# Kernel tuning notes

Measured on AMD Instinct MI355X. Metric: run time of the kernel, lower is better.

The kernel has to match this reference:

```python
import jax, jax.numpy as jnp
import numpy as np

EPS_BN = 1e-5


def _batchnorm(h, g, b):
    # training-mode BatchNorm1d over the flattened (B*N*k) axis
    mu = jnp.mean(h, axis=0)
    var = jnp.var(h, axis=0)
    return g * (h - mu) * jax.lax.rsqrt(var + EPS_BN) + b


def setup_inputs() -> dict:
    key = jax.random.key(0)
    ks = jax.random.split(key, 5)
    B, N = 4, 8192
    x = jax.random.normal(ks[0], (B, N, 3), dtype=jnp.float32)
    W1 = jax.random.normal(ks[1], (7, 10), dtype=jnp.float32) * (1.0 / np.sqrt(7.0))
    b1 = jax.random.normal(ks[2], (10,), dtype=jnp.float32) * 0.01
    W2 = jax.random.normal(ks[3], (10, 10), dtype=jnp.float32) * (1.0 / np.sqrt(10.0))
    b2 = jax.random.normal(ks[4], (10,), dtype=jnp.float32) * 0.01
    g1 = jnp.ones((10,), jnp.float32); be1 = jnp.zeros((10,), jnp.float32)
    g2 = jnp.ones((10,), jnp.float32); be2 = jnp.zeros((10,), jnp.float32)
    return {"x": x, "W1": W1, "b1": b1, "g1": g1, "be1": be1,
            "W2": W2, "b2": b2, "g2": g2, "be2": be2, "k": 9}


def reference(x, W1, b1, g1, be1, W2, b2, g2, be2, k):
    B, N, C = x.shape
    # --- kNN graph (brute force, self included as nearest) ---
    sq = jnp.sum(x * x, axis=-1)                                    # (B,N)
    d2 = sq[:, :, None] + sq[:, None, :] - 2.0 * jnp.einsum('bnc,bmc->bnm', x, x)
    _, idx = jax.lax.top_k(-d2, k + 1)                              # (B,N,k+1)
    nbrs = x[jnp.arange(B)[:, None, None], idx]                     # (B,N,k+1,3)
    rel = (nbrs - x[:, :, None, :])[:, :, 1:, :]                    # drop self -> (B,N,k,3)
    # --- sort neighbors by azimuth phi = atan2(y, x) ---
    phi = jnp.arctan2(rel[..., 1], rel[..., 0])                     # (B,N,k)
    order = jnp.argsort(phi, axis=-1)
    v1 = jnp.take_along_axis(rel, order[..., None], axis=2)         # (B,N,k,3)
    v2 = jnp.roll(v1, -1, axis=2)                                   # next neighbor (cyclic)
    # --- umbrella-style surface features ---
    centroids = 0.5 * (v1 + v2)
    normals = jnp.cross(v1, v2)
    normals = normals / (jnp.linalg.norm(normals, axis=-1, keepdims=True) + 1e-6)
    sign = jnp.where(normals[..., 0:1, 0] > 0, 1.0, -1.0)[..., None]  # (B,N,1,1)
    normals = normals * sign
    position = jnp.sum(normals * centroids, axis=-1, keepdims=True) / jnp.sqrt(jnp.asarray(3.0, x.dtype))
    feat = jnp.concatenate([centroids, normals, position], axis=-1)   # (B,N,k,7)
    feat = feat.reshape(B * N * k, 7)
    # --- tiny MLP + max-pool over k ---
    h = jax.nn.relu(_batchnorm(feat @ W1 + b1, g1, be1))
    h = jax.nn.relu(_batchnorm(h @ W2 + b2, g2, be2))
    return jnp.max(h.reshape(B, N, k, 10), axis=2)                  # (B,N,10)
```

## Files before the change

kernel.cpp:

```cpp
#include <hip/hip_runtime.h>
#include <math.h>
#include <float.h>
#include <stdint.h>

#define B_ 4
#define N_ 8192
#define K_ 9
#define NPTS (B_ * N_)
#define NROWS (NPTS * K_)
#define SPLIT 8
#define CHUNK (N_ / SPLIT)
#define NGROUP 32
#define GSIZE (CHUNK / NGROUP)
#define GSTRIDE 33

__device__ __forceinline__ float dist2f(float4 q, float4 c) {
  float dot = q.x * c.x + q.y * c.y + q.z * c.z;
  return (q.w + c.w) - 2.0f * dot;
}

#define GDECL(G) float gd##G; int gi##G;
#define SCANG(G)                                                           \
  { float bgd = FLT_MAX; int bgi = 0;                                      \
    _Pragma("clang loop unroll(disable)")                                  \
    for (int jj = 0; jj < GSIZE; jj += 4) {                                \
      const float4* cp = CH + (G * GSTRIDE + jj);                          \
      float4 c0 = cp[0], c1 = cp[1], c2 = cp[2], c3 = cp[3];               \
      int j = G * GSIZE + jj;                                              \
      float d0 = dist2f(q, c0), d1 = dist2f(q, c1);                        \
      float d2 = dist2f(q, c2), d3 = dist2f(q, c3);                        \
      if (HS) {                                                            \
        d0 = (j + 0 == nl) ? FLT_MAX : d0;                                 \
        d1 = (j + 1 == nl) ? FLT_MAX : d1;                                 \
        d2 = (j + 2 == nl) ? FLT_MAX : d2;                                 \
        d3 = (j + 3 == nl) ? FLT_MAX : d3;                                 \
      }                                                                    \
      bool l0 = d0 < bgd; bgd = l0 ? d0 : bgd; bgi = l0 ? (j + 0) : bgi;   \
      bool l1 = d1 < bgd; bgd = l1 ? d1 : bgd; bgi = l1 ? (j + 1) : bgi;   \
      bool l2 = d2 < bgd; bgd = l2 ? d2 : bgd; bgi = l2 ? (j + 2) : bgi;   \
      bool l3 = d3 < bgd; bgd = l3 ? d3 : bgd; bgi = l3 ? (j + 3) : bgi;   \
    }                                                                      \
    gd##G = bgd; gi##G = bgi; }
#define LM(G)                                                              \
  { bool lt = gd##G < wd;                                                  \
    wd = lt ? gd##G : wd; wi = lt ? gi##G : wi; wg = lt ? G : wg; }
#define WBK(G)                                                             \
  { bool m = (wg == G); gd##G = m ? nd : gd##G; gi##G = m ? ni : gi##G; }

template <bool HS>
__device__ __forceinline__ void knn_chunk(const float4* CH, float4 q, int nl,
                                          int j0, int s, int p,
                                          uint2* __restrict__ PBDI) {
  GDECL(0) GDECL(1) GDECL(2) GDECL(3) GDECL(4) GDECL(5) GDECL(6) GDECL(7)
  GDECL(8) GDECL(9) GDECL(10) GDECL(11) GDECL(12) GDECL(13) GDECL(14) GDECL(15)
  GDECL(16) GDECL(17) GDECL(18) GDECL(19) GDECL(20) GDECL(21) GDECL(22) GDECL(23)
  GDECL(24) GDECL(25) GDECL(26) GDECL(27) GDECL(28) GDECL(29) GDECL(30) GDECL(31)

  SCANG(0) SCANG(1) SCANG(2) SCANG(3) SCANG(4) SCANG(5) SCANG(6) SCANG(7)
  SCANG(8) SCANG(9) SCANG(10) SCANG(11) SCANG(12) SCANG(13) SCANG(14) SCANG(15)
  SCANG(16) SCANG(17) SCANG(18) SCANG(19) SCANG(20) SCANG(21) SCANG(22) SCANG(23)
  SCANG(24) SCANG(25) SCANG(26) SCANG(27) SCANG(28) SCANG(29) SCANG(30) SCANG(31)

#pragma clang loop unroll(disable)
  for (int r = 0; r < K_; ++r) {
    float wd = gd0; int wi = gi0; int wg = 0;
    LM(1) LM(2) LM(3) LM(4) LM(5) LM(6) LM(7)
    LM(8) LM(9) LM(10) LM(11) LM(12) LM(13) LM(14) LM(15)
    LM(16) LM(17) LM(18) LM(19) LM(20) LM(21) LM(22) LM(23)
    LM(24) LM(25) LM(26) LM(27) LM(28) LM(29) LM(30) LM(31)
    uint2 o; o.x = __float_as_uint(wd); o.y = (unsigned)(j0 + wi);
    PBDI[(size_t)(s * K_ + r) * NPTS + p] = o;

    int ab = wg * GSTRIDE;
    int jb = wg * GSIZE;
    float nd = FLT_MAX; int ni = 0;
#pragma clang loop unroll(disable)
    for (int jj = 0; jj < GSIZE; jj += 4) {
      const float4* cp = CH + (ab + jj);
      float4 c0 = cp[0], c1 = cp[1], c2 = cp[2], c3 = cp[3];
      int j = jb + jj;
      float d0 = dist2f(q, c0), d1 = dist2f(q, c1);
      float d2 = dist2f(q, c2), d3 = dist2f(q, c3);
      if (HS) {
        d0 = (j + 0 == nl) ? FLT_MAX : d0;
        d1 = (j + 1 == nl) ? FLT_MAX : d1;
        d2 = (j + 2 == nl) ? FLT_MAX : d2;
        d3 = (j + 3 == nl) ? FLT_MAX : d3;
      }
      bool k0 = (d0 > wd) | ((d0 == wd) & ((j + 0) > wi));
      bool k1 = (d1 > wd) | ((d1 == wd) & ((j + 1) > wi));
      bool k2 = (d2 > wd) | ((d2 == wd) & ((j + 2) > wi));
      bool k3 = (d3 > wd) | ((d3 == wd) & ((j + 3) > wi));
      d0 = k0 ? d0 : FLT_MAX;
      d1 = k1 ? d1 : FLT_MAX;
      d2 = k2 ? d2 : FLT_MAX;
      d3 = k3 ? d3 : FLT_MAX;
      bool l0 = d0 < nd; nd = l0 ? d0 : nd; ni = l0 ? (j + 0) : ni;
      bool l1 = d1 < nd; nd = l1 ? d1 : nd; ni = l1 ? (j + 1) : ni;
      bool l2 = d2 < nd; nd = l2 ? d2 : nd; ni = l2 ? (j + 2) : ni;
      bool l3 = d3 < nd; nd = l3 ? d3 : nd; ni = l3 ? (j + 3) : ni;
    }
    WBK(0) WBK(1) WBK(2) WBK(3) WBK(4) WBK(5) WBK(6) WBK(7)
    WBK(8) WBK(9) WBK(10) WBK(11) WBK(12) WBK(13) WBK(14) WBK(15)
    WBK(16) WBK(17) WBK(18) WBK(19) WBK(20) WBK(21) WBK(22) WBK(23)
    WBK(24) WBK(25) WBK(26) WBK(27) WBK(28) WBK(29) WBK(30) WBK(31)
  }
}

__launch_bounds__(128, 4)
__global__ void k_knn(const float* __restrict__ x, uint2* __restrict__ PBDI) {
  __shared__ float4 CH[NGROUP * GSTRIDE];
  int bid = blockIdx.x;
  int pg = bid >> 3;
  int s = bid & (SPLIT - 1);
  int p = pg * 128 + threadIdx.x;
  int b = p >> 13;
  int n = p & (N_ - 1);
  int bO = b * N_;
  int j0 = s * CHUNK;

  const float* xq = x + 3 * (size_t)p;
  float qa = xq[0], qb = xq[1], qc = xq[2];
  float4 q = make_float4(qa, qb, qc, qa * qa + qb * qb + qc * qc);

  for (int t = threadIdx.x; t < CHUNK; t += 128) {
    const float* xp = x + 3 * (size_t)(bO + j0 + t);
    float a = xp[0], bb = xp[1], cc = xp[2];
    CH[(t >> 5) * GSTRIDE + (t & 31)] = make_float4(a, bb, cc, a * a + bb * bb + cc * cc);
  }
  __syncthreads();

  int n0 = (pg * 128) & (N_ - 1);
  int nl = n - j0;
  if (s == (n0 >> 10)) knn_chunk<true >(CH, q, nl, j0, s, p, PBDI);
  else                 knn_chunk<false>(CH, q, nl, j0, s, p, PBDI);
}

#define LVL(bdv, biv)                                                     \
  { bool lt = cd < (bdv); float td = (bdv); int ti = (biv);               \
    (bdv) = lt ? cd : (bdv); (biv) = lt ? ci : (biv);                     \
    cd = lt ? td : cd; ci = lt ? ti : ci; }
#define INS9ALL()                                                         \
  LVL(b0d, b0i) LVL(b1d, b1i) LVL(b2d, b2i) LVL(b3d, b3i) LVL(b4d, b4i)  \
  LVL(b5d, b5i) LVL(b6d, b6i) LVL(b7d, b7i) LVL(b8d, b8i)
#define TOP9_DECL()                                                       \
  float b0d = FLT_MAX, b1d = FLT_MAX, b2d = FLT_MAX, b3d = FLT_MAX,       \
        b4d = FLT_MAX, b5d = FLT_MAX, b6d = FLT_MAX, b7d = FLT_MAX,       \
        b8d = FLT_MAX;                                                    \
  int b0i = 0, b1i = 0, b2i = 0, b3i = 0, b4i = 0, b5i = 0, b6i = 0,      \
      b7i = 0, b8i = 0;

#define MKREL(T)                                                          \
  float rx##T, ry##T, rz##T, ph##T;                                       \
  { const float* mp = x + 3 * (size_t)(bO + b##T##i);                     \
    rx##T = mp[0] - qa; ry##T = mp[1] - qb; rz##T = mp[2] - qc;           \
    ph##T = atan2f(ry##T, rx##T); }

#define CE(A, Bv)                                                         \
  { bool lt = ph##Bv < ph##A; float t0;                                   \
    t0 = ph##A; ph##A = lt ? ph##Bv : t0; ph##Bv = lt ? t0 : ph##Bv;      \
    t0 = rx##A; rx##A = lt ? rx##Bv : t0; rx##Bv = lt ? t0 : rx##Bv;      \
    t0 = ry##A; ry##A = lt ? ry##Bv : t0; ry##Bv = lt ? t0 : ry##Bv;      \
    t0 = rz##A; rz##A = lt ? rz##Bv : t0; rz##Bv = lt ? t0 : rz##Bv; }

#define ST9(arr, v0, v1, v2, v3, v4, v5, v6, v7, v8)                      \
  arr[0 * 64 + pl] = v0; arr[1 * 64 + pl] = v1; arr[2 * 64 + pl] = v2;    \
  arr[3 * 64 + pl] = v3; arr[4 * 64 + pl] = v4; arr[5 * 64 + pl] = v5;    \
  arr[6 * 64 + pl] = v6; arr[7 * 64 + pl] = v7; arr[8 * 64 + pl] = v8;

__launch_bounds__(256, 4)
__global__ void k_tail1(const float* __restrict__ x, const uint2* __restrict__ PBDI,
                        const float* __restrict__ W1, const float* __restrict__ b1,
                        float* __restrict__ H1, double* __restrict__ ACC1) {
  __shared__ float  LMD[64 * 37];
  __shared__ int    LMI[64 * 37];
  __shared__ float  LREL[3][9 * 64];
  __shared__ float  LSGN[64];
  __shared__ double sred[4][20];

  int q = threadIdx.x >> 6;
  int pl = threadIdx.x & 63;
  int pbase = blockIdx.x * 64;
  int p = pbase + pl;

  {
    TOP9_DECL();
#pragma clang loop unroll_count(2)
    for (int e = 0; e < 2 * K_; ++e) {
      uint2 v = PBDI[(size_t)(q * 2 * K_ + e) * NPTS + p];
      float cd = __uint_as_float(v.x);
      int ci = (int)v.y;
      INS9ALL();
    }
    int base = pl * 37 + q * 9;
    LMD[base + 0] = b0d; LMD[base + 1] = b1d; LMD[base + 2] = b2d;
    LMD[base + 3] = b3d; LMD[base + 4] = b4d; LMD[base + 5] = b5d;
    LMD[base + 6] = b6d; LMD[base + 7] = b7d; LMD[base + 8] = b8d;
    LMI[base + 0] = b0i; LMI[base + 1] = b1i; LMI[base + 2] = b2i;
    LMI[base + 3] = b3i; LMI[base + 4] = b4i; LMI[base + 5] = b5i;
    LMI[base + 6] = b6i; LMI[base + 7] = b7i; LMI[base + 8] = b8i;
  }
  __syncthreads();

  if (q == 0) {
    int b = p >> 13;
    int bO = b * N_;
    const float* xq = x + 3 * (size_t)p;
    float qa = xq[0], qb = xq[1], qc = xq[2];

    TOP9_DECL();
#pragma clang loop unroll_count(3)
    for (int e = 0; e < 4 * K_; ++e) {
      float cd = LMD[pl * 37 + e];
      int ci = LMI[pl * 37 + e];
      INS9ALL();
    }

    MKREL(0) MKREL(1) MKREL(2) MKREL(3) MKREL(4)
    MKREL(5) MKREL(6) MKREL(7) MKREL(8)

    CE(0,1)
    CE(1,2) CE(0,1)
    CE(2,3) CE(1,2) CE(0,1)
    CE(3,4) CE(2,3) CE(1,2) CE(0,1)
    CE(4,5) CE(3,4) CE(2,3) CE(1,2) CE(0,1)
    CE(5,6) CE(4,5) CE(3,4) CE(2,3) CE(1,2) CE(0,1)
    CE(6,7) CE(5,6) CE(4,5) CE(3,4) CE(2,3) CE(1,2) CE(0,1)
    CE(7,8) CE(6,7) CE(5,6) CE(4,5) CE(3,4) CE(2,3) CE(1,2) CE(0,1)

    float nx0 = ry0 * rz1 - rz0 * ry1;
    float ny0 = rz0 * rx1 - rx0 * rz1;
    float nz0 = rx0 * ry1 - ry0 * rx1;
    float nrm0 = sqrtf(nx0 * nx0 + ny0 * ny0 + nz0 * nz0) + 1e-6f;
    LSGN[pl] = ((nx0 / nrm0) > 0.0f) ? 1.0f : -1.0f;

    ST9(LREL[0], rx0, rx1, rx2, rx3, rx4, rx5, rx6, rx7, rx8)
    ST9(LREL[1], ry0, ry1, ry2, ry3, ry4, ry5, ry6, ry7, ry8)
    ST9(LREL[2], rz0, rz1, rz2, rz3, rz4, rz5, rz6, rz7, rz8)
  }
  __syncthreads();

  double sum[10], ss[10];
#pragma unroll
  for (int c = 0; c < 10; ++c) { sum[c] = 0.0; ss[c] = 0.0; }

#pragma clang loop unroll(disable)
  for (int rl = threadIdx.x; rl < 9 * 64; rl += 256) {
    int t = rl >> 6;
    int pp = rl & 63;
    int t2 = (t + 1 == K_) ? 0 : t + 1;
    float v1x = LREL[0][t * 64 + pp];
    float v1y = LREL[1][t * 64 + pp];
    float v1z = LREL[2][t * 64 + pp];
    float v2x = LREL[0][t2 * 64 + pp];
    float v2y = LREL[1][t2 * 64 + pp];
    float v2z = LREL[2][t2 * 64 + pp];
    float sgn = LSGN[pp];

    float cx = 0.5f * (v1x + v2x);
    float cy = 0.5f * (v1y + v2y);
    float cz = 0.5f * (v1z + v2z);
    float nx = v1y * v2z - v1z * v2y;
    float ny = v1z * v2x - v1x * v2z;
    float nz = v1x * v2y - v1y * v2x;
    float nrm = sqrtf(nx * nx + ny * ny + nz * nz) + 1e-6f;
    nx /= nrm; ny /= nrm; nz /= nrm;
    nx *= sgn; ny *= sgn; nz *= sgn;
    float pos = (nx * cx + ny * cy + nz * cz) / 1.7320508075688772f;

    float fv[7] = {cx, cy, cz, nx, ny, nz, pos};
#pragma unroll
    for (int c = 0; c < 10; ++c) {
      float h = b1[c];
#pragma unroll
      for (int rr = 0; rr < 7; ++rr) h = fmaf(fv[rr], W1[rr * 10 + c], h);
      H1[(size_t)c * NROWS + (size_t)t * NPTS + pbase + pp] = h;
      double hd = (double)h;
      sum[c] += hd; ss[c] += hd * hd;
    }
  }

  int lane = threadIdx.x & 63, wv = threadIdx.x >> 6;
#pragma unroll
  for (int c = 0; c < 10; ++c) {
    double a = sum[c];
#pragma unroll
    for (int off = 32; off > 0; off >>= 1) a += __shfl_down(a, off);
    if (lane == 0) sred[wv][c] = a;
    double qq = ss[c];
#pragma unroll
    for (int off = 32; off > 0; off >>= 1) qq += __shfl_down(qq, off);
    if (lane == 0) sred[wv][10 + c] = qq;
  }
  __syncthreads();
  if (threadIdx.x < 20) {
    atomicAdd(&ACC1[threadIdx.x],
              sred[0][threadIdx.x] + sred[1][threadIdx.x] +
              sred[2][threadIdx.x] + sred[3][threadIdx.x]);
  }
}

__launch_bounds__(256)
__global__ void k_mlp2(const float* __restrict__ H1, const double* __restrict__ ACC1,
                       const float* __restrict__ g1, const float* __restrict__ be1,
                       const float* __restrict__ W2, const float* __restrict__ b2,
                       float* __restrict__ H2, double* __restrict__ ACC2) {
  __shared__ float MR[20];
  if (threadIdx.x < 10) {
    double mu = ACC1[threadIdx.x] / (double)NROWS;
    double var = ACC1[10 + threadIdx.x] / (double)NROWS - mu * mu;
    MR[threadIdx.x] = (float)mu;
    MR[10 + threadIdx.x] = (float)(1.0 / sqrt(var + 1e-5));
  }
  __syncthreads();

  int r = blockIdx.x * 256 + threadIdx.x;
  float v[10];
#pragma unroll
  for (int c = 0; c < 10; ++c) {
    float h = H1[(size_t)c * NROWS + r];
    float z = g1[c] * (h - MR[c]) * MR[10 + c] + be1[c];
    v[c] = z > 0.0f ? z : 0.0f;
  }
  float o[10];
#pragma unroll
  for (int c = 0; c < 10; ++c) {
    float h = b2[c];
#pragma unroll
    for (int t = 0; t < 10; ++t) h = fmaf(v[t], W2[t * 10 + c], h);
    o[c] = h;
    H2[(size_t)c * NROWS + r] = h;
  }

  __shared__ double sred[4][20];
  int lane = threadIdx.x & 63, wv = threadIdx.x >> 6;
#pragma unroll
  for (int c = 0; c < 10; ++c) {
    double a = (double)o[c];
#pragma unroll
    for (int off = 32; off > 0; off >>= 1) a += __shfl_down(a, off);
    if (lane == 0) sred[wv][c] = a;
    double qq = (double)o[c] * (double)o[c];
#pragma unroll
    for (int off = 32; off > 0; off >>= 1) qq += __shfl_down(qq, off);
    if (lane == 0) sred[wv][10 + c] = qq;
  }
  __syncthreads();
  if (threadIdx.x < 20) {
    atomicAdd(&ACC2[threadIdx.x],
              sred[0][threadIdx.x] + sred[1][threadIdx.x] +
              sred[2][threadIdx.x] + sred[3][threadIdx.x]);
  }
}

__launch_bounds__(256)
__global__ void k_out(const float* __restrict__ H2, const double* __restrict__ ACC2,
                      const float* __restrict__ g2, const float* __restrict__ be2,
                      float* __restrict__ out) {
  __shared__ float MR[20];
  if (threadIdx.x < 10) {
    double mu = ACC2[threadIdx.x] / (double)NROWS;
    double var = ACC2[10 + threadIdx.x] / (double)NROWS - mu * mu;
    MR[threadIdx.x] = (float)mu;
    MR[10 + threadIdx.x] = (float)(1.0 / sqrt(var + 1e-5));
  }
  __syncthreads();

  int p = blockIdx.x * 256 + threadIdx.x;
#pragma unroll
  for (int c = 0; c < 10; ++c) {
    float m = -FLT_MAX;
#pragma unroll
    for (int j = 0; j < K_; ++j) {
      float h = H2[(size_t)c * NROWS + j * NPTS + p];
      float z = g2[c] * (h - MR[c]) * MR[10 + c] + be2[c];
      z = z > 0.0f ? z : 0.0f;
      m = fmaxf(m, z);
    }
    out[(size_t)p * 10 + c] = m;
  }
}

extern "C" void kernel_launch(void* const* d_in, const int* in_sizes, int n_in,
                              void* d_out, int out_size, void* d_ws, size_t ws_size,
                              hipStream_t stream) {
  (void)in_sizes; (void)n_in; (void)out_size; (void)ws_size;
  const float* x  = (const float*)d_in[0];
  const float* W1 = (const float*)d_in[1];
  const float* b1 = (const float*)d_in[2];
  const float* g1 = (const float*)d_in[3];
  const float* be1= (const float*)d_in[4];
  const float* W2 = (const float*)d_in[5];
  const float* b2 = (const float*)d_in[6];
  const float* g2 = (const float*)d_in[7];
  const float* be2= (const float*)d_in[8];
  float* out = (float*)d_out;

  char* base = (char*)d_ws;
  uint2*  PBDI = (uint2*)base;
  float*  H1 = (float*)(base + (size_t)SPLIT * K_ * NPTS * 8);
  double* ACC = (double*)(H1 + (size_t)10 * NROWS);
  double* ACC1 = ACC;
  double* ACC2 = ACC + 20;
  float*  H2 = (float*)PBDI;

  hipMemsetAsync(ACC, 0, 40 * sizeof(double), stream);
  k_knn<<<(NPTS / 128) * SPLIT, 128, 0, stream>>>(x, PBDI);
  k_tail1<<<NPTS / 64, 256, 0, stream>>>(x, PBDI, W1, b1, H1, ACC1);
  k_mlp2<<<NROWS / 256, 256, 0, stream>>>(H1, ACC1, g1, be1, W2, b2, H2, ACC2);
  k_out<<<NPTS / 256, 256, 0, stream>>>(H2, ACC2, g2, be2, out);
}
```

Before: 258.7 us.

## Halve kNN split count, widen groups, split BN atomics across copies

The kNN kernel now splits each point's candidates into 4 chunks instead of 8, using 64 groups per chunk. The per-round argmin runs as four parallel chains and the group rescan as two. The merge in k_tail1 drops its two-level shared-memory reduction and reads the 36 partial candidates straight from global memory. BatchNorm statistics accumulate into 16 replicated double accumulators to reduce atomic contention, which the consumers sum. Each thread holds 64 group registers and occupancy is lowered (launch bounds 128,2), so register pressure and fewer blocks per CU are the risks.

```diff
diff --git a/kernel.cpp b/kernel.cpp
--- a/kernel.cpp
+++ b/kernel.cpp
@@ -8,11 +8,12 @@
 #define K_ 9
 #define NPTS (B_ * N_)
 #define NROWS (NPTS * K_)
-#define SPLIT 8
+#define SPLIT 4
 #define CHUNK (N_ / SPLIT)
-#define NGROUP 32
+#define NGROUP 64
 #define GSIZE (CHUNK / NGROUP)
 #define GSTRIDE 33
+#define NCOPY 16
 
 __device__ __forceinline__ float dist2f(float4 q, float4 c) {
   float dot = q.x * c.x + q.y * c.y + q.z * c.z;
@@ -41,9 +42,13 @@
       bool l3 = d3 < bgd; bgd = l3 ? d3 : bgd; bgi = l3 ? (j + 3) : bgi;   \
     }                                                                      \
     gd##G = bgd; gi##G = bgi; }
-#define LM(G)                                                              \
-  { bool lt = gd##G < wd;                                                  \
-    wd = lt ? gd##G : wd; wi = lt ? gi##G : wi; wg = lt ? G : wg; }
+#define LMC(G, S)                                                          \
+  { bool lt = gd##G < wd##S;                                               \
+    wd##S = lt ? gd##G : wd##S; wi##S = lt ? gi##G : wi##S;                \
+    wg##S = lt ? G : wg##S; }
+#define CMB(S)                                                             \
+  { bool lt = wd##S < wda;                                                 \
+    wda = lt ? wd##S : wda; wia = lt ? wi##S : wia; wga = lt ? wg##S : wga; }
 #define WBK(G)                                                             \
   { bool m = (wg == G); gd##G = m ? nd : gd##G; gi##G = m ? ni : gi##G; }
 
@@ -55,27 +60,46 @@
   GDECL(8) GDECL(9) GDECL(10) GDECL(11) GDECL(12) GDECL(13) GDECL(14) GDECL(15)
   GDECL(16) GDECL(17) GDECL(18) GDECL(19) GDECL(20) GDECL(21) GDECL(22) GDECL(23)
   GDECL(24) GDECL(25) GDECL(26) GDECL(27) GDECL(28) GDECL(29) GDECL(30) GDECL(31)
+  GDECL(32) GDECL(33) GDECL(34) GDECL(35) GDECL(36) GDECL(37) GDECL(38) GDECL(39)
+  GDECL(40) GDECL(41) GDECL(42) GDECL(43) GDECL(44) GDECL(45) GDECL(46) GDECL(47)
+  GDECL(48) GDECL(49) GDECL(50) GDECL(51) GDECL(52) GDECL(53) GDECL(54) GDECL(55)
+  GDECL(56) GDECL(57) GDECL(58) GDECL(59) GDECL(60) GDECL(61) GDECL(62) GDECL(63)
 
   SCANG(0) SCANG(1) SCANG(2) SCANG(3) SCANG(4) SCANG(5) SCANG(6) SCANG(7)
   SCANG(8) SCANG(9) SCANG(10) SCANG(11) SCANG(12) SCANG(13) SCANG(14) SCANG(15)
   SCANG(16) SCANG(17) SCANG(18) SCANG(19) SCANG(20) SCANG(21) SCANG(22) SCANG(23)
   SCANG(24) SCANG(25) SCANG(26) SCANG(27) SCANG(28) SCANG(29) SCANG(30) SCANG(31)
+  SCANG(32) SCANG(33) SCANG(34) SCANG(35) SCANG(36) SCANG(37) SCANG(38) SCANG(39)
+  SCANG(40) SCANG(41) SCANG(42) SCANG(43) SCANG(44) SCANG(45) SCANG(46) SCANG(47)
+  SCANG(48) SCANG(49) SCANG(50) SCANG(51) SCANG(52) SCANG(53) SCANG(54) SCANG(55)
+  SCANG(56) SCANG(57) SCANG(58) SCANG(59) SCANG(60) SCANG(61) SCANG(62) SCANG(63)
 
 #pragma clang loop unroll(disable)
   for (int r = 0; r < K_; ++r) {
-    float wd = gd0; int wi = gi0; int wg = 0;
-    LM(1) LM(2) LM(3) LM(4) LM(5) LM(6) LM(7)
-    LM(8) LM(9) LM(10) LM(11) LM(12) LM(13) LM(14) LM(15)
-    LM(16) LM(17) LM(18) LM(19) LM(20) LM(21) LM(22) LM(23)
-    LM(24) LM(25) LM(26) LM(27) LM(28) LM(29) LM(30) LM(31)
+    float wda = gd0; int wia = gi0; int wga = 0;
+    LMC(1,a) LMC(2,a) LMC(3,a) LMC(4,a) LMC(5,a) LMC(6,a) LMC(7,a)
+    LMC(8,a) LMC(9,a) LMC(10,a) LMC(11,a) LMC(12,a) LMC(13,a) LMC(14,a) LMC(15,a)
+    float wdb = gd16; int wib = gi16; int wgb = 16;
+    LMC(17,b) LMC(18,b) LMC(19,b) LMC(20,b) LMC(21,b) LMC(22,b) LMC(23,b)
+    LMC(24,b) LMC(25,b) LMC(26,b) LMC(27,b) LMC(28,b) LMC(29,b) LMC(30,b) LMC(31,b)
+    float wdc = gd32; int wic = gi32; int wgc = 32;
+    LMC(33,c) LMC(34,c) LMC(35,c) LMC(36,c) LMC(37,c) LMC(38,c) LMC(39,c)
+    LMC(40,c) LMC(41,c) LMC(42,c) LMC(43,c) LMC(44,c) LMC(45,c) LMC(46,c) LMC(47,c)
+    float wdd = gd48; int wid = gi48; int wgd = 48;
+    LMC(49,d) LMC(50,d) LMC(51,d) LMC(52,d) LMC(53,d) LMC(54,d) LMC(55,d)
+    LMC(56,d) LMC(57,d) LMC(58,d) LMC(59,d) LMC(60,d) LMC(61,d) LMC(62,d) LMC(63,d)
+    CMB(b) CMB(c) CMB(d)
+    float wd = wda; int wi = wia; int wg = wga;
+
     uint2 o; o.x = __float_as_uint(wd); o.y = (unsigned)(j0 + wi);
     PBDI[(size_t)(s * K_ + r) * NPTS + p] = o;
 
     int ab = wg * GSTRIDE;
     int jb = wg * GSIZE;
-    float nd = FLT_MAX; int ni = 0;
+    float ndA = FLT_MAX; int niA = 0;
+    float ndB = FLT_MAX; int niB = 0;
 #pragma clang loop unroll(disable)
-    for (int jj = 0; jj < GSIZE; jj += 4) {
+    for (int jj = 0; jj < GSIZE / 2; jj += 4) {
       const float4* cp = CH + (ab + jj);
       float4 c0 = cp[0], c1 = cp[1], c2 = cp[2], c3 = cp[3];
       int j = jb + jj;
@@ -95,23 +119,56 @@
       d1 = k1 ? d1 : FLT_MAX;
       d2 = k2 ? d2 : FLT_MAX;
       d3 = k3 ? d3 : FLT_MAX;
-      bool l0 = d0 < nd; nd = l0 ? d0 : nd; ni = l0 ? (j + 0) : ni;
-      bool l1 = d1 < nd; nd = l1 ? d1 : nd; ni = l1 ? (j + 1) : ni;
-      bool l2 = d2 < nd; nd = l2 ? d2 : nd; ni = l2 ? (j + 2) : ni;
-      bool l3 = d3 < nd; nd = l3 ? d3 : nd; ni = l3 ? (j + 3) : ni;
-    }
+      bool l0 = d0 < ndA; ndA = l0 ? d0 : ndA; niA = l0 ? (j + 0) : niA;
+      bool l1 = d1 < ndA; ndA = l1 ? d1 : ndA; niA = l1 ? (j + 1) : niA;
+      bool l2 = d2 < ndA; ndA = l2 ? d2 : ndA; niA = l2 ? (j + 2) : niA;
+      bool l3 = d3 < ndA; ndA = l3 ? d3 : ndA; niA = l3 ? (j + 3) : niA;
+    }
+#pragma clang loop unroll(disable)
+    for (int jj = GSIZE / 2; jj < GSIZE; jj += 4) {
+      const float4* cp = CH + (ab + jj);
+      float4 c0 = cp[0], c1 = cp[1], c2 = cp[2], c3 = cp[3];
+      int j = jb + jj;
+      float d0 = dist2f(q, c0), d1 = dist2f(q, c1);
+      float d2 = dist2f(q, c2), d3 = dist2f(q, c3);
+      if (HS) {
+        d0 = (j + 0 == nl) ? FLT_MAX : d0;
+        d1 = (j + 1 == nl) ? FLT_MAX : d1;
+        d2 = (j + 2 == nl) ? FLT_MAX : d2;
+        d3 = (j + 3 == nl) ? FLT_MAX : d3;
+      }
+      bool k0 = (d0 > wd) | ((d0 == wd) & ((j + 0) > wi));
+      bool k1 = (d1 > wd) | ((d1 == wd) & ((j + 1) > wi));
+      bool k2 = (d2 > wd) | ((d2 == wd) & ((j + 2) > wi));
+      bool k3 = (d3 > wd) | ((d3 == wd) & ((j + 3) > wi));
+      d0 = k0 ? d0 : FLT_MAX;
+      d1 = k1 ? d1 : FLT_MAX;
+      d2 = k2 ? d2 : FLT_MAX;
+      d3 = k3 ? d3 : FLT_MAX;
+      bool l0 = d0 < ndB; ndB = l0 ? d0 : ndB; niB = l0 ? (j + 0) : niB;
+      bool l1 = d1 < ndB; ndB = l1 ? d1 : ndB; niB = l1 ? (j + 1) : niB;
+      bool l2 = d2 < ndB; ndB = l2 ? d2 : ndB; niB = l2 ? (j + 2) : niB;
+      bool l3 = d3 < ndB; ndB = l3 ? d3 : ndB; niB = l3 ? (j + 3) : niB;
+    }
+    bool ltB = ndB < ndA;
+    float nd = ltB ? ndB : ndA; int ni = ltB ? niB : niA;
+
     WBK(0) WBK(1) WBK(2) WBK(3) WBK(4) WBK(5) WBK(6) WBK(7)
     WBK(8) WBK(9) WBK(10) WBK(11) WBK(12) WBK(13) WBK(14) WBK(15)
     WBK(16) WBK(17) WBK(18) WBK(19) WBK(20) WBK(21) WBK(22) WBK(23)
     WBK(24) WBK(25) WBK(26) WBK(27) WBK(28) WBK(29) WBK(30) WBK(31)
-  }
-}
-
-__launch_bounds__(128, 4)
+    WBK(32) WBK(33) WBK(34) WBK(35) WBK(36) WBK(37) WBK(38) WBK(39)
+    WBK(40) WBK(41) WBK(42) WBK(43) WBK(44) WBK(45) WBK(46) WBK(47)
+    WBK(48) WBK(49) WBK(50) WBK(51) WBK(52) WBK(53) WBK(54) WBK(55)
+    WBK(56) WBK(57) WBK(58) WBK(59) WBK(60) WBK(61) WBK(62) WBK(63)
+  }
+}
+
+__launch_bounds__(128, 2)
 __global__ void k_knn(const float* __restrict__ x, uint2* __restrict__ PBDI) {
   __shared__ float4 CH[NGROUP * GSTRIDE];
   int bid = blockIdx.x;
-  int pg = bid >> 3;
+  int pg = bid >> 2;
   int s = bid & (SPLIT - 1);
   int p = pg * 128 + threadIdx.x;
   int b = p >> 13;
@@ -132,7 +189,7 @@
 
   int n0 = (pg * 128) & (N_ - 1);
   int nl = n - j0;
-  if (s == (n0 >> 10)) knn_chunk<true >(CH, q, nl, j0, s, p, PBDI);
+  if (s == (n0 >> 11)) knn_chunk<true >(CH, q, nl, j0, s, p, PBDI);
   else                 knn_chunk<false>(CH, q, nl, j0, s, p, PBDI);
 }
 
@@ -171,9 +228,7 @@
 __launch_bounds__(256, 4)
 __global__ void k_tail1(const float* __restrict__ x, const uint2* __restrict__ PBDI,
                         const float* __restrict__ W1, const float* __restrict__ b1,
-                        float* __restrict__ H1, double* __restrict__ ACC1) {
-  __shared__ float  LMD[64 * 37];
-  __shared__ int    LMI[64 * 37];
+                        float* __restrict__ H1, double* __restrict__ ACC) {
   __shared__ float  LREL[3][9 * 64];
   __shared__ float  LSGN[64];
   __shared__ double sred[4][20];
@@ -182,25 +237,6 @@
   int pl = threadIdx.x & 63;
   int pbase = blockIdx.x * 64;
   int p = pbase + pl;
-
-  {
-    TOP9_DECL();
-#pragma clang loop unroll_count(2)
-    for (int e = 0; e < 2 * K_; ++e) {
-      uint2 v = PBDI[(size_t)(q * 2 * K_ + e) * NPTS + p];
-      float cd = __uint_as_float(v.x);
-      int ci = (int)v.y;
-      INS9ALL();
-    }
-    int base = pl * 37 + q * 9;
-    LMD[base + 0] = b0d; LMD[base + 1] = b1d; LMD[base + 2] = b2d;
-    LMD[base + 3] = b3d; LMD[base + 4] = b4d; LMD[base + 5] = b5d;
-    LMD[base + 6] = b6d; LMD[base + 7] = b7d; LMD[base + 8] = b8d;
-    LMI[base + 0] = b0i; LMI[base + 1] = b1i; LMI[base + 2] = b2i;
-    LMI[base + 3] = b3i; LMI[base + 4] = b4i; LMI[base + 5] = b5i;
-    LMI[base + 6] = b6i; LMI[base + 7] = b7i; LMI[base + 8] = b8i;
-  }
-  __syncthreads();
 
   if (q == 0) {
     int b = p >> 13;
@@ -209,10 +245,11 @@
     float qa = xq[0], qb = xq[1], qc = xq[2];
 
     TOP9_DECL();
-#pragma clang loop unroll_count(3)
-    for (int e = 0; e < 4 * K_; ++e) {
-      float cd = LMD[pl * 37 + e];
-      int ci = LMI[pl * 37 + e];
+#pragma clang loop unroll_count(4)
+    for (int e = 0; e < SPLIT * K_; ++e) {
+      uint2 v = PBDI[(size_t)e * NPTS + p];
+      float cd = __uint_as_float(v.x);
+      int ci = (int)v.y;
       INS9ALL();
     }
 
@@ -294,21 +331,27 @@
   }
   __syncthreads();
   if (threadIdx.x < 20) {
-    atomicAdd(&ACC1[threadIdx.x],
+    atomicAdd(&ACC[(blockIdx.x & (NCOPY - 1)) * 40 + threadIdx.x],
               sred[0][threadIdx.x] + sred[1][threadIdx.x] +
               sred[2][threadIdx.x] + sred[3][threadIdx.x]);
   }
 }
 
 __launch_bounds__(256)
-__global__ void k_mlp2(const float* __restrict__ H1, const double* __restrict__ ACC1,
+__global__ void k_mlp2(const float* __restrict__ H1, double* __restrict__ ACC,
                        const float* __restrict__ g1, const float* __restrict__ be1,
                        const float* __restrict__ W2, const float* __restrict__ b2,
-                       float* __restrict__ H2, double* __restrict__ ACC2) {
+                       float* __restrict__ H2) {
   __shared__ float MR[20];
   if (threadIdx.x < 10) {
-    double mu = ACC1[threadIdx.x] / (double)NROWS;
-    double var = ACC1[10 + threadIdx.x] / (double)NROWS - mu * mu;
+    double s0 = 0.0, s1 = 0.0;
+#pragma unroll
+    for (int cc = 0; cc < NCOPY; ++cc) {
+      s0 += ACC[cc * 40 + threadIdx.x];
+      s1 += ACC[cc * 40 + 10 + threadIdx.x];
+    }
+    double mu = s0 / (double)NROWS;
+    double var = s1 / (double)NROWS - mu * mu;
     MR[threadIdx.x] = (float)mu;
     MR[10 + threadIdx.x] = (float)(1.0 / sqrt(var + 1e-5));
   }
@@ -347,20 +390,26 @@
   }
   __syncthreads();
   if (threadIdx.x < 20) {
-    atomicAdd(&ACC2[threadIdx.x],
+    atomicAdd(&ACC[(blockIdx.x & (NCOPY - 1)) * 40 + 20 + threadIdx.x],
               sred[0][threadIdx.x] + sred[1][threadIdx.x] +
               sred[2][threadIdx.x] + sred[3][threadIdx.x]);
   }
 }
 
 __launch_bounds__(256)
-__global__ void k_out(const float* __restrict__ H2, const double* __restrict__ ACC2,
+__global__ void k_out(const float* __restrict__ H2, const double* __restrict__ ACC,
                       const float* __restrict__ g2, const float* __restrict__ be2,
                       float* __restrict__ out) {
   __shared__ float MR[20];
   if (threadIdx.x < 10) {
-    double mu = ACC2[threadIdx.x] / (double)NROWS;
-    double var = ACC2[10 + threadIdx.x] / (double)NROWS - mu * mu;
+    double s0 = 0.0, s1 = 0.0;
+#pragma unroll
+    for (int cc = 0; cc < NCOPY; ++cc) {
+      s0 += ACC[cc * 40 + 20 + threadIdx.x];
+      s1 += ACC[cc * 40 + 30 + threadIdx.x];
+    }
+    double mu = s0 / (double)NROWS;
+    double var = s1 / (double)NROWS - mu * mu;
     MR[threadIdx.x] = (float)mu;
     MR[10 + threadIdx.x] = (float)(1.0 / sqrt(var + 1e-5));
   }
@@ -397,16 +446,15 @@
   float* out = (float*)d_out;
 
   char* base = (char*)d_ws;
+  size_t R0 = (size_t)10 * NROWS * 4;
   uint2*  PBDI = (uint2*)base;
-  float*  H1 = (float*)(base + (size_t)SPLIT * K_ * NPTS * 8);
-  double* ACC = (double*)(H1 + (size_t)10 * NROWS);
-  double* ACC1 = ACC;
-  double* ACC2 = ACC + 20;
-  float*  H2 = (float*)PBDI;
-
-  hipMemsetAsync(ACC, 0, 40 * sizeof(double), stream);
+  float*  H2 = (float*)base;
+  float*  H1 = (float*)(base + R0);
+  double* ACC = (double*)(base + 2 * R0);
+
+  hipMemsetAsync(ACC, 0, NCOPY * 40 * sizeof(double), stream);
   k_knn<<<(NPTS / 128) * SPLIT, 128, 0, stream>>>(x, PBDI);
-  k_tail1<<<NPTS / 64, 256, 0, stream>>>(x, PBDI, W1, b1, H1, ACC1);
-  k_mlp2<<<NROWS / 256, 256, 0, stream>>>(H1, ACC1, g1, be1, W2, b2, H2, ACC2);
-  k_out<<<NPTS / 256, 256, 0, stream>>>(H2, ACC2, g2, be2, out);
-}
+  k_tail1<<<NPTS / 64, 256, 0, stream>>>(x, PBDI, W1, b1, H1, ACC);
+  k_mlp2<<<NROWS / 256, 256, 0, stream>>>(H1, ACC, g1, be1, W2, b2, H2);
+  k_out<<<NPTS / 256, 256, 0, stream>>>(H2, ACC, g2, be2, out);
+}
```

Measured after the change: 264.0 us. 2.0% more time.
